# Optimization experiments

Hardware: AMD Instinct MI355X
Metric: run time of the kernel (lower is better)

## Reference

```python
import jax, jax.numpy as jnp
import numpy as np

N_NODES = 50000
N_EDGES = 800000
D_IN = 96
HID = 128
N_GRAPHS = 256


def _lin_init(key, fan_out, fan_in):
    # torch Linear default: U(-1/sqrt(fan_in), 1/sqrt(fan_in))
    bound = 1.0 / np.sqrt(fan_in)
    return jax.random.uniform(key, (fan_out, fan_in), jnp.float32, -bound, bound)


def setup_inputs() -> dict:
    key = jax.random.key(0)
    ks = jax.random.split(key, 14)
    x = jax.random.normal(ks[0], (N_NODES, D_IN), jnp.float32)
    edge_index = jax.random.randint(ks[1], (2, N_EDGES), 0, N_NODES)
    batch = jnp.sort(jax.random.randint(ks[2], (N_NODES,), 0, N_GRAPHS))
    edge_attr = jax.random.uniform(ks[3], (N_EDGES,), jnp.float32)
    # conv1: GraphConv(D_IN, HID)
    W_rel1 = _lin_init(ks[4], HID, D_IN)
    b_rel1 = jnp.zeros((HID,), jnp.float32)
    W_root1 = _lin_init(ks[5], HID, D_IN)
    # conv3: GraphConv(HID, HID)
    W_rel3 = _lin_init(ks[6], HID, HID)
    b_rel3 = jnp.zeros((HID,), jnp.float32)
    W_root3 = _lin_init(ks[7], HID, HID)
    # lin: Linear(HID, 1)
    W_lin = _lin_init(ks[8], 1, HID)
    b_lin = jnp.zeros((1,), jnp.float32)
    return {"x": x, "edge_index": edge_index, "batch": batch, "edge_attr": edge_attr,
            "W_rel1": W_rel1, "b_rel1": b_rel1, "W_root1": W_root1,
            "W_rel3": W_rel3, "b_rel3": b_rel3, "W_root3": W_root3,
            "W_lin": W_lin, "b_lin": b_lin}


def _graph_conv(h, src, dst, w_edge, W_rel, b_rel, W_root):
    # PyG GraphConv (aggr='add'): out_i = W_rel @ sum_{j->i} e_ji * h_j + b_rel + W_root @ h_i
    msg = h[src] * w_edge[:, None]                       # [E, F] gather + scale
    agg = jax.ops.segment_sum(msg, dst, num_segments=N_NODES)  # [N, F]
    return agg @ W_rel.T + b_rel + h @ W_root.T


def reference(x, edge_index, batch, edge_attr,
              W_rel1, b_rel1, W_root1,
              W_rel3, b_rel3, W_root3,
              W_lin, b_lin):
    src, dst = edge_index[0], edge_index[1]  # source_to_target flow
    h = jax.nn.relu(_graph_conv(x, src, dst, edge_attr, W_rel1, b_rel1, W_root1))
    # dropout(p=0.5) is identity in eval mode
    h = _graph_conv(h, src, dst, edge_attr, W_rel3, b_rel3, W_root3)
    # global_mean_pool over graph ids
    sums = jax.ops.segment_sum(h, batch, num_segments=N_GRAPHS)          # [G, HID]
    counts = jax.ops.segment_sum(jnp.ones((N_NODES,), h.dtype), batch,
                                 num_segments=N_GRAPHS)                  # [G]
    pooled = sums / jnp.maximum(counts, 1.0)[:, None]
    return jax.nn.relu(pooled @ W_lin.T + b_lin)  # [G, 1]
```

## Files before the change

kernel.cpp:

```cpp
#include <hip/hip_runtime.h>
#include <hip/hip_fp16.h>

constexpr int NN  = 50000;
constexpr int NE  = 800000;
constexpr int DIN = 96;
constexpr int HID = 128;
constexpr int NG  = 256;

constexpr int CAP = 48;

constexpr int NBF = (NE + 511) / 512;
constexpr int NCV = (NN * DIN / 8 + 511) / 512;
constexpr int NTR = (2 * HID * DIN + 511) / 512;
constexpr int NB3 = (NN + 255) / 256;

constexpr int NZ  = 4 + 2 * NG + NN;

static __device__ inline unsigned h2u(__half2 h) {
    union { __half2 h; unsigned u; } c; c.h = h; return c.u;
}

__launch_bounds__(512)
__global__ void zero_kernel(int* __restrict__ zbase) {
    int i = blockIdx.x * 512 + threadIdx.x;
    if (i < NZ / 4) ((int4*)zbase)[i] = make_int4(0, 0, 0, 0);
}

__launch_bounds__(512)
__global__ void build_kernel(const float* __restrict__ x,
                             const int* __restrict__ ei,
                             const float* __restrict__ ea,
                             const float* __restrict__ Wrel1,
                             const float* __restrict__ Wroot1,
                             const float* __restrict__ Wrel3,
                             const float* __restrict__ Wroot3,
                             const float* __restrict__ Wlin,
                             const float* __restrict__ b3,
                             float* __restrict__ WrelT,
                             float* __restrict__ WrootT,
                             float* __restrict__ u, float* __restrict__ v,
                             float* __restrict__ c0,
                             int* __restrict__ deg,
                             unsigned* __restrict__ bucket,
                             __half* __restrict__ x16) {
    const int b = blockIdx.x, tid = threadIdx.x;
    if (b < NBF) {
        int e = b * 512 + tid;
        if (e < NE) {
            int dst = ei[NE + e];
            int slot = atomicAdd(&deg[dst], 1);
            if (slot < CAP) {
                unsigned wq = __float2uint_rz(ea[e] * 65536.0f);
                wq = wq > 65535u ? 65535u : wq;
                bucket[(size_t)dst * CAP + slot] = ((unsigned)ei[e] << 16) | wq;
            }
        }
    } else if (b < NBF + NCV) {
        int j = (b - NBF) * 512 + tid;
        if (j < NN * DIN / 8) {
            float4 a = ((const float4*)x)[2 * j];
            float4 c = ((const float4*)x)[2 * j + 1];
            uint4 o;
            o.x = h2u(__floats2half2_rn(a.x, a.y));
            o.y = h2u(__floats2half2_rn(a.z, a.w));
            o.z = h2u(__floats2half2_rn(c.x, c.y));
            o.w = h2u(__floats2half2_rn(c.z, c.w));
            ((uint4*)x16)[j] = o;
        }
    } else if (b < NBF + NCV + NTR) {
        int i = (b - NBF - NCV) * 512 + tid;
        int n = HID * DIN;
        const float* src = (i < n) ? Wrel1 : Wroot1;
        float* dst       = (i < n) ? WrelT : WrootT;
        int j = (i < n) ? i : i - n;
        int r = j / DIN, c = j - r * DIN;
        dst[c * HID + r] = src[j];
    } else {
        __shared__ float pu[4][HID];
        __shared__ float pv[4][HID];
        __shared__ float pc[HID];
        int k = tid & 127;
        int qtr = tid >> 7;
        float su = 0.f, sv = 0.f;
        for (int f = qtr * 32; f < qtr * 32 + 32; ++f) {
            float wl = Wlin[f];
            su = fmaf(wl, Wrel3[f * HID + k], su);
            sv = fmaf(wl, Wroot3[f * HID + k], sv);
        }
        pu[qtr][k] = su;
        pv[qtr][k] = sv;
        if (qtr == 0) pc[k] = Wlin[k] * b3[k];
        __syncthreads();
        if (qtr == 0) {
            u[k] = pu[0][k] + pu[1][k] + pu[2][k] + pu[3][k];
            v[k] = pv[0][k] + pv[1][k] + pv[2][k] + pv[3][k];
        }
        if (tid == 0) {
            float c = 0.f;
            for (int f = 0; f < HID; ++f) c += pc[f];
            c0[0] = c;
        }
    }
}

__launch_bounds__(256)
__global__ void fused_conv1_kernel(const __half* __restrict__ x16,
                                   const int* __restrict__ deg,
                                   const unsigned* __restrict__ bucket,
                                   const float* __restrict__ WrelT,
                                   const float* __restrict__ WrootT,
                                   const float* __restrict__ brel,
                                   const float* __restrict__ u,
                                   const float* __restrict__ v,
                                   float* __restrict__ p,
                                   float* __restrict__ q) {
    __shared__ __align__(16) __half sxh[32][DIN];
    __shared__ __align__(16) float  sa[32][DIN];
    const int tid = threadIdx.x;
    const int nn = tid >> 5;
    const int fq = tid & 31;
    const int base = blockIdx.x * 32;
    const int n0 = nn * 4;
    const bool ld = (fq < 24);

    for (int j = tid; j < 32 * 12; j += 256) {
        int node = j / 12;
        int r = j - node * 12;
        int n = base + node;
        if (n < NN) {
            ((uint4*)sxh[node])[r] = ((const uint4*)(x16 + (size_t)n * DIN))[r];
            ((uint4*)sa[node])[r]  = ((const uint4*)(bucket + (size_t)n * CAP))[r];
        }
    }
    __syncthreads();

    for (int c = 0; c < 4; ++c) {
        int n = base + n0 + c;
        if (n >= NN) break;
        int cnt = deg[n];
        cnt = cnt < CAP ? cnt : CAP;
        const unsigned* rrow = (const unsigned*)sa[n0 + c];
        float4 aA = make_float4(0.f, 0.f, 0.f, 0.f);
        float4 aB = make_float4(0.f, 0.f, 0.f, 0.f);
        constexpr float S = 1.0f / 65536.0f;
        int t = 0;
        int full = cnt & ~7;
        for (; t < full; t += 8) {
            unsigned r0 = rrow[t + 0], r1 = rrow[t + 1];
            unsigned r2 = rrow[t + 2], r3 = rrow[t + 3];
            unsigned r4 = rrow[t + 4], r5 = rrow[t + 5];
            unsigned r6 = rrow[t + 6], r7 = rrow[t + 7];
            float w0 = ((r0 & 0xffffu) + 0.5f) * S;
            float w1 = ((r1 & 0xffffu) + 0.5f) * S;
            float w2 = ((r2 & 0xffffu) + 0.5f) * S;
            float w3 = ((r3 & 0xffffu) + 0.5f) * S;
            float w4 = ((r4 & 0xffffu) + 0.5f) * S;
            float w5 = ((r5 & 0xffffu) + 0.5f) * S;
            float w6 = ((r6 & 0xffffu) + 0.5f) * S;
            float w7 = ((r7 & 0xffffu) + 0.5f) * S;
            if (ld) {
                uint2 g0 = ((const uint2*)(x16 + (size_t)(r0 >> 16) * DIN))[fq];
                uint2 g1 = ((const uint2*)(x16 + (size_t)(r1 >> 16) * DIN))[fq];
                uint2 g2 = ((const uint2*)(x16 + (size_t)(r2 >> 16) * DIN))[fq];
                uint2 g3 = ((const uint2*)(x16 + (size_t)(r3 >> 16) * DIN))[fq];
                uint2 g4 = ((const uint2*)(x16 + (size_t)(r4 >> 16) * DIN))[fq];
                uint2 g5 = ((const uint2*)(x16 + (size_t)(r5 >> 16) * DIN))[fq];
                uint2 g6 = ((const uint2*)(x16 + (size_t)(r6 >> 16) * DIN))[fq];
                uint2 g7 = ((const uint2*)(x16 + (size_t)(r7 >> 16) * DIN))[fq];
#define EFMA(ACC, W, G)                                                       \
                {                                                             \
                    float2 f01 = __half22float2(*(__half2*)&G.x);             \
                    float2 f23 = __half22float2(*(__half2*)&G.y);             \
                    ACC.x = fmaf(W, f01.x, ACC.x);                            \
                    ACC.y = fmaf(W, f01.y, ACC.y);                            \
                    ACC.z = fmaf(W, f23.x, ACC.z);                            \
                    ACC.w = fmaf(W, f23.y, ACC.w);                            \
                }
                EFMA(aA, w0, g0) EFMA(aB, w1, g1)
                EFMA(aA, w2, g2) EFMA(aB, w3, g3)
                EFMA(aA, w4, g4) EFMA(aB, w5, g5)
                EFMA(aA, w6, g6) EFMA(aB, w7, g7)
            }
        }
        if (t < cnt) {
            unsigned r0, r1, r2, r3, r4, r5, r6, r7;
#define EREC(I) r##I = rrow[(t + I < cnt) ? t + I : t];
            EREC(0) EREC(1) EREC(2) EREC(3) EREC(4) EREC(5) EREC(6) EREC(7)
#undef EREC
            float w0 = (t + 0 < cnt) ? ((r0 & 0xffffu) + 0.5f) * S : 0.f;
            float w1 = (t + 1 < cnt) ? ((r1 & 0xffffu) + 0.5f) * S : 0.f;
            float w2 = (t + 2 < cnt) ? ((r2 & 0xffffu) + 0.5f) * S : 0.f;
            float w3 = (t + 3 < cnt) ? ((r3 & 0xffffu) + 0.5f) * S : 0.f;
            float w4 = (t + 4 < cnt) ? ((r4 & 0xffffu) + 0.5f) * S : 0.f;
            float w5 = (t + 5 < cnt) ? ((r5 & 0xffffu) + 0.5f) * S : 0.f;
            float w6 = (t + 6 < cnt) ? ((r6 & 0xffffu) + 0.5f) * S : 0.f;
            float w7 = (t + 7 < cnt) ? ((r7 & 0xffffu) + 0.5f) * S : 0.f;
            if (ld) {
                uint2 g0 = ((const uint2*)(x16 + (size_t)(r0 >> 16) * DIN))[fq];
                uint2 g1 = ((const uint2*)(x16 + (size_t)(r1 >> 16) * DIN))[fq];
                uint2 g2 = ((const uint2*)(x16 + (size_t)(r2 >> 16) * DIN))[fq];
                uint2 g3 = ((const uint2*)(x16 + (size_t)(r3 >> 16) * DIN))[fq];
                uint2 g4 = ((const uint2*)(x16 + (size_t)(r4 >> 16) * DIN))[fq];
                uint2 g5 = ((const uint2*)(x16 + (size_t)(r5 >> 16) * DIN))[fq];
                uint2 g6 = ((const uint2*)(x16 + (size_t)(r6 >> 16) * DIN))[fq];
                uint2 g7 = ((const uint2*)(x16 + (size_t)(r7 >> 16) * DIN))[fq];
                EFMA(aA, w0, g0) EFMA(aB, w1, g1)
                EFMA(aA, w2, g2) EFMA(aB, w3, g3)
                EFMA(aA, w4, g4) EFMA(aB, w5, g5)
                EFMA(aA, w6, g6) EFMA(aB, w7, g7)
#undef EFMA
            }
        }
        if (ld) {
            float4 a4v = make_float4(aA.x + aB.x, aA.y + aB.y,
                                     aA.z + aB.z, aA.w + aB.w);
            *(float4*)&sa[n0 + c][fq * 4] = a4v;
        }
    }
    __syncthreads();

    float4 b4 = ((const float4*)brel)[fq];
    float4 acc0 = b4, acc1 = b4, acc2 = b4, acc3 = b4;

    for (int k = 0; k < DIN; k += 4) {
        float4 wr0 = ((const float4*)WrelT)[(k + 0) * 32 + fq];
        float4 wr1 = ((const float4*)WrelT)[(k + 1) * 32 + fq];
        float4 wr2 = ((const float4*)WrelT)[(k + 2) * 32 + fq];
        float4 wr3 = ((const float4*)WrelT)[(k + 3) * 32 + fq];
        float4 wo0 = ((const float4*)WrootT)[(k + 0) * 32 + fq];
        float4 wo1 = ((const float4*)WrootT)[(k + 1) * 32 + fq];
        float4 wo2 = ((const float4*)WrootT)[(k + 2) * 32 + fq];
        float4 wo3 = ((const float4*)WrootT)[(k + 3) * 32 + fq];
#define CSTEP(ACC, NODE)                                                      \
        {                                                                     \
            float4 a = *(const float4*)&sa[NODE][k];                          \
            uint2 bb = *(const uint2*)&sxh[NODE][k];                          \
            float2 b01 = __half22float2(*(const __half2*)&bb.x);              \
            float2 b23 = __half22float2(*(const __half2*)&bb.y);              \
            ACC.x = fmaf(a.x, wr0.x, ACC.x); ACC.x = fmaf(a.y, wr1.x, ACC.x); \
            ACC.x = fmaf(a.z, wr2.x, ACC.x); ACC.x = fmaf(a.w, wr3.x, ACC.x); \
            ACC.x = fmaf(b01.x, wo0.x, ACC.x); ACC.x = fmaf(b01.y, wo1.x, ACC.x); \
            ACC.x = fmaf(b23.x, wo2.x, ACC.x); ACC.x = fmaf(b23.y, wo3.x, ACC.x); \
            ACC.y = fmaf(a.x, wr0.y, ACC.y); ACC.y = fmaf(a.y, wr1.y, ACC.y); \
            ACC.y = fmaf(a.z, wr2.y, ACC.y); ACC.y = fmaf(a.w, wr3.y, ACC.y); \
            ACC.y = fmaf(b01.x, wo0.y, ACC.y); ACC.y = fmaf(b01.y, wo1.y, ACC.y); \
            ACC.y = fmaf(b23.x, wo2.y, ACC.y); ACC.y = fmaf(b23.y, wo3.y, ACC.y); \
            ACC.z = fmaf(a.x, wr0.z, ACC.z); ACC.z = fmaf(a.y, wr1.z, ACC.z); \
            ACC.z = fmaf(a.z, wr2.z, ACC.z); ACC.z = fmaf(a.w, wr3.z, ACC.z); \
            ACC.z = fmaf(b01.x, wo0.z, ACC.z); ACC.z = fmaf(b01.y, wo1.z, ACC.z); \
            ACC.z = fmaf(b23.x, wo2.z, ACC.z); ACC.z = fmaf(b23.y, wo3.z, ACC.z); \
            ACC.w = fmaf(a.x, wr0.w, ACC.w); ACC.w = fmaf(a.y, wr1.w, ACC.w); \
            ACC.w = fmaf(a.z, wr2.w, ACC.w); ACC.w = fmaf(a.w, wr3.w, ACC.w); \
            ACC.w = fmaf(b01.x, wo0.w, ACC.w); ACC.w = fmaf(b01.y, wo1.w, ACC.w); \
            ACC.w = fmaf(b23.x, wo2.w, ACC.w); ACC.w = fmaf(b23.y, wo3.w, ACC.w); \
        }
        CSTEP(acc0, n0 + 0)
        CSTEP(acc1, n0 + 1)
        CSTEP(acc2, n0 + 2)
        CSTEP(acc3, n0 + 3)
#undef CSTEP
    }

    float4 u4 = ((const float4*)u)[fq];
    float4 v4 = ((const float4*)v)[fq];
#define EPI(ACC, C)                                                            \
    {                                                                          \
        ACC.x = fmaxf(ACC.x, 0.f); ACC.y = fmaxf(ACC.y, 0.f);                  \
        ACC.z = fmaxf(ACC.z, 0.f); ACC.w = fmaxf(ACC.w, 0.f);                  \
        float pp = ACC.x * u4.x + ACC.y * u4.y + ACC.z * u4.z + ACC.w * u4.w;  \
        float qq = ACC.x * v4.x + ACC.y * v4.y + ACC.z * v4.z + ACC.w * v4.w;  \
        for (int off = 16; off > 0; off >>= 1) {                               \
            pp += __shfl_xor(pp, off, 32);                                     \
            qq += __shfl_xor(qq, off, 32);                                     \
        }                                                                      \
        int n = base + n0 + C;                                                 \
        if (fq == 0 && n < NN) { p[n] = pp; q[n] = qq; }                       \
    }
    EPI(acc0, 0)
    EPI(acc1, 1)
    EPI(acc2, 2)
    EPI(acc3, 3)
#undef EPI
}

__launch_bounds__(256)
__global__ void finalize_kernel(const int* __restrict__ deg,
                                const unsigned* __restrict__ bucket,
                                const float* __restrict__ p,
                                const float* __restrict__ q,
                                const int* __restrict__ batch,
                                float* __restrict__ gaccE,
                                float* __restrict__ gaccC,
                                int* __restrict__ counter,
                                const float* __restrict__ c0,
                                const float* __restrict__ blin,
                                float* __restrict__ out) {
    __shared__ float lb[NG];
    __shared__ float lc[NG];
    int tid = threadIdx.x;
    lb[tid] = 0.f;
    lc[tid] = 0.f;
    __syncthreads();
    int n = blockIdx.x * 256 + tid;
    if (n < NN) {
        int cnt = deg[n];
        cnt = cnt < CAP ? cnt : CAP;
        const unsigned* row = bucket + (size_t)n * CAP;
        constexpr float S = 1.0f / 65536.0f;
        float E = 0.f;
        int t = 0;
        for (; t + 4 <= cnt; t += 4) {
            unsigned r0 = row[t + 0], r1 = row[t + 1];
            unsigned r2 = row[t + 2], r3 = row[t + 3];
            float p0 = p[r0 >> 16], p1 = p[r1 >> 16];
            float p2 = p[r2 >> 16], p3 = p[r3 >> 16];
            E = fmaf(((r0 & 0xffffu) + 0.5f) * S, p0, E);
            E = fmaf(((r1 & 0xffffu) + 0.5f) * S, p1, E);
            E = fmaf(((r2 & 0xffffu) + 0.5f) * S, p2, E);
            E = fmaf(((r3 & 0xffffu) + 0.5f) * S, p3, E);
        }
        for (; t < cnt; ++t) {
            unsigned r = row[t];
            E = fmaf(((r & 0xffffu) + 0.5f) * S, p[r >> 16], E);
        }
        int g = batch[n];
        atomicAdd(&lb[g], E + q[n]);
        atomicAdd(&lc[g], 1.f);
    }
    __syncthreads();
    atomicAdd(&gaccE[tid], lb[tid]);
    atomicAdd(&gaccC[tid], lc[tid]);
    __threadfence();
    __shared__ int sticket;
    if (tid == 0) sticket = atomicAdd(counter, 1);
    __syncthreads();
    if (sticket == NB3 - 1) {
        __threadfence();
        float accE = gaccE[tid];
        float nf   = gaccC[tid];
        float val = (accE + nf * c0[0]) / fmaxf(nf, 1.f) + blin[0];
        out[tid] = fmaxf(val, 0.f);
    }
}

extern "C" void kernel_launch(void* const* d_in, const int* in_sizes, int n_in,
                              void* d_out, int out_size, void* d_ws, size_t ws_size,
                              hipStream_t stream) {
    const float* x      = (const float*)d_in[0];
    const int*   ei     = (const int*)  d_in[1];
    const int*   batch  = (const int*)  d_in[2];
    const float* ea     = (const float*)d_in[3];
    const float* Wrel1  = (const float*)d_in[4];
    const float* brel1  = (const float*)d_in[5];
    const float* Wroot1 = (const float*)d_in[6];
    const float* Wrel3  = (const float*)d_in[7];
    const float* brel3  = (const float*)d_in[8];
    const float* Wroot3 = (const float*)d_in[9];
    const float* Wlin   = (const float*)d_in[10];
    const float* blin   = (const float*)d_in[11];
    float* out = (float*)d_out;

    float* ws = (float*)d_ws;
    float* WrelT1   = ws;
    float* WrootT1  = WrelT1 + DIN * HID;
    float* u        = WrootT1 + DIN * HID;
    float* v        = u + HID;
    float* c0       = v + HID;
    float* p        = c0 + 8;
    float* q        = p + 50048;
    float* zbase    = q + 50048;
    int*   counter  = (int*)zbase;
    float* gaccE    = zbase + 4;
    float* gaccC    = gaccE + NG;
    int*   deg      = (int*)(gaccC + NG);
    unsigned* bucket = (unsigned*)(deg + NN);
    __half* x16     = (__half*)(bucket + (size_t)NN * CAP);

    zero_kernel<<<(NZ / 4 + 511) / 512, 512, 0, stream>>>((int*)zbase);

    build_kernel<<<NBF + NCV + NTR + 1, 512, 0, stream>>>(
        x, ei, ea, Wrel1, Wroot1, Wrel3, Wroot3, Wlin, brel3,
        WrelT1, WrootT1, u, v, c0, deg, bucket, x16);

    fused_conv1_kernel<<<(NN + 31) / 32, 256, 0, stream>>>(
        x16, deg, bucket, WrelT1, WrootT1, brel1, u, v, p, q);

    finalize_kernel<<<NB3, 256, 0, stream>>>(
        deg, bucket, p, q, batch, gaccE, gaccC, counter, c0, blin, out);
}
```

Baseline: 230.5 us.

## Split finalize gathers across 8 lanes per node and move graph counts to build

The finalize kernel now assigns 8 lanes per node, each taking a strided slice of the bucket row, and combines them with width-8 shuffles. One lane per node then adds to the global per-graph accumulator directly, with no shared-memory staging. Per-graph node counts move into new blocks of the build kernel. The edge bucketing is also reworked so each thread handles two edges, giving more loads and atomics in flight. Together these aim to hide gather latency in finalize. In exchange they add global atomic contention on 256 graph slots and launch eight times as many finalize blocks.

```diff
diff --git a/kernel.cpp b/kernel.cpp
--- a/kernel.cpp
+++ b/kernel.cpp
@@ -9,10 +9,12 @@
 
 constexpr int CAP = 48;
 
-constexpr int NBF = (NE + 511) / 512;
+constexpr int NEH = NE / 2;
+constexpr int NBF = (NEH + 511) / 512;
 constexpr int NCV = (NN * DIN / 8 + 511) / 512;
 constexpr int NTR = (2 * HID * DIN + 511) / 512;
-constexpr int NB3 = (NN + 255) / 256;
+constexpr int NHG = (NN + 511) / 512;
+constexpr int NB4 = (NN * 8 + 255) / 256;
 
 constexpr int NZ  = 4 + 2 * NG + NN;
 
@@ -30,6 +32,7 @@
 __global__ void build_kernel(const float* __restrict__ x,
                              const int* __restrict__ ei,
                              const float* __restrict__ ea,
+                             const int* __restrict__ batch,
                              const float* __restrict__ Wrel1,
                              const float* __restrict__ Wroot1,
                              const float* __restrict__ Wrel3,
@@ -42,17 +45,27 @@
                              float* __restrict__ c0,
                              int* __restrict__ deg,
                              unsigned* __restrict__ bucket,
-                             __half* __restrict__ x16) {
+                             __half* __restrict__ x16,
+                             float* __restrict__ gaccC) {
     const int b = blockIdx.x, tid = threadIdx.x;
     if (b < NBF) {
-        int e = b * 512 + tid;
-        if (e < NE) {
-            int dst = ei[NE + e];
-            int slot = atomicAdd(&deg[dst], 1);
-            if (slot < CAP) {
-                unsigned wq = __float2uint_rz(ea[e] * 65536.0f);
+        int i = b * 512 + tid;
+        if (i < NEH) {
+            int e0 = i, e1 = i + NEH;
+            int d0 = ei[NE + e0];
+            int d1 = ei[NE + e1];
+            float a0 = ea[e0], a1 = ea[e1];
+            int s0 = atomicAdd(&deg[d0], 1);
+            int s1 = atomicAdd(&deg[d1], 1);
+            if (s0 < CAP) {
+                unsigned wq = __float2uint_rz(a0 * 65536.0f);
                 wq = wq > 65535u ? 65535u : wq;
-                bucket[(size_t)dst * CAP + slot] = ((unsigned)ei[e] << 16) | wq;
+                bucket[(size_t)d0 * CAP + s0] = ((unsigned)ei[e0] << 16) | wq;
+            }
+            if (s1 < CAP) {
+                unsigned wq = __float2uint_rz(a1 * 65536.0f);
+                wq = wq > 65535u ? 65535u : wq;
+                bucket[(size_t)d1 * CAP + s1] = ((unsigned)ei[e1] << 16) | wq;
             }
         }
     } else if (b < NBF + NCV) {
@@ -75,6 +88,9 @@
         int j = (i < n) ? i : i - n;
         int r = j / DIN, c = j - r * DIN;
         dst[c * HID + r] = src[j];
+    } else if (b < NBF + NCV + NTR + NHG) {
+        int i = (b - NBF - NCV - NTR) * 512 + tid;
+        if (i < NN) atomicAdd(&gaccC[batch[i]], 1.0f);
     } else {
         __shared__ float pu[4][HID];
         __shared__ float pv[4][HID];
@@ -290,51 +306,36 @@
                                 const float* __restrict__ q,
                                 const int* __restrict__ batch,
                                 float* __restrict__ gaccE,
-                                float* __restrict__ gaccC,
+                                const float* __restrict__ gaccC,
                                 int* __restrict__ counter,
                                 const float* __restrict__ c0,
                                 const float* __restrict__ blin,
                                 float* __restrict__ out) {
-    __shared__ float lb[NG];
-    __shared__ float lc[NG];
-    int tid = threadIdx.x;
-    lb[tid] = 0.f;
-    lc[tid] = 0.f;
-    __syncthreads();
-    int n = blockIdx.x * 256 + tid;
+    const int tid = threadIdx.x;
+    const int t = blockIdx.x * 256 + tid;
+    const int n = t >> 3;
+    const int s0 = t & 7;
     if (n < NN) {
         int cnt = deg[n];
         cnt = cnt < CAP ? cnt : CAP;
         const unsigned* row = bucket + (size_t)n * CAP;
         constexpr float S = 1.0f / 65536.0f;
         float E = 0.f;
-        int t = 0;
-        for (; t + 4 <= cnt; t += 4) {
-            unsigned r0 = row[t + 0], r1 = row[t + 1];
-            unsigned r2 = row[t + 2], r3 = row[t + 3];
-            float p0 = p[r0 >> 16], p1 = p[r1 >> 16];
-            float p2 = p[r2 >> 16], p3 = p[r3 >> 16];
-            E = fmaf(((r0 & 0xffffu) + 0.5f) * S, p0, E);
-            E = fmaf(((r1 & 0xffffu) + 0.5f) * S, p1, E);
-            E = fmaf(((r2 & 0xffffu) + 0.5f) * S, p2, E);
-            E = fmaf(((r3 & 0xffffu) + 0.5f) * S, p3, E);
-        }
-        for (; t < cnt; ++t) {
-            unsigned r = row[t];
+        for (int s = s0; s < cnt; s += 8) {
+            unsigned r = row[s];
             E = fmaf(((r & 0xffffu) + 0.5f) * S, p[r >> 16], E);
         }
-        int g = batch[n];
-        atomicAdd(&lb[g], E + q[n]);
-        atomicAdd(&lc[g], 1.f);
-    }
+        E += __shfl_xor(E, 4, 8);
+        E += __shfl_xor(E, 2, 8);
+        E += __shfl_xor(E, 1, 8);
+        if (s0 == 0) atomicAdd(&gaccE[batch[n]], E + q[n]);
+    }
+    __threadfence();
     __syncthreads();
-    atomicAdd(&gaccE[tid], lb[tid]);
-    atomicAdd(&gaccC[tid], lc[tid]);
-    __threadfence();
     __shared__ int sticket;
     if (tid == 0) sticket = atomicAdd(counter, 1);
     __syncthreads();
-    if (sticket == NB3 - 1) {
+    if (sticket == NB4 - 1) {
         __threadfence();
         float accE = gaccE[tid];
         float nf   = gaccC[tid];
@@ -378,13 +379,13 @@
 
     zero_kernel<<<(NZ / 4 + 511) / 512, 512, 0, stream>>>((int*)zbase);
 
-    build_kernel<<<NBF + NCV + NTR + 1, 512, 0, stream>>>(
-        x, ei, ea, Wrel1, Wroot1, Wrel3, Wroot3, Wlin, brel3,
-        WrelT1, WrootT1, u, v, c0, deg, bucket, x16);
+    build_kernel<<<NBF + NCV + NTR + NHG + 1, 512, 0, stream>>>(
+        x, ei, ea, batch, Wrel1, Wroot1, Wrel3, Wroot3, Wlin, brel3,
+        WrelT1, WrootT1, u, v, c0, deg, bucket, x16, gaccC);
 
     fused_conv1_kernel<<<(NN + 31) / 32, 256, 0, stream>>>(
         x16, deg, bucket, WrelT1, WrootT1, brel1, u, v, p, q);
 
-    finalize_kernel<<<NB3, 256, 0, stream>>>(
+    finalize_kernel<<<NB4, 256, 0, stream>>>(
         deg, bucket, p, q, batch, gaccE, gaccC, counter, c0, blin, out);
 }
```

New measurement: 431.4 us. 87.1% more time.
